# Performance work log

Hardware: AMD Instinct MI355X
Metric: run time of the kernel (lower is better)

The kernel has to match this reference:

```python
import jax, jax.numpy as jnp
import numpy as np

N_ENT = 15000  # entity id range; also used for relation ids in this synthetic setup

def _triple_key(h, r, t):
    # Unique int64 key per (h, r, t) triple; max ~15000^3 < 2^63.
    return (h * N_ENT + r) * N_ENT + t

def setup_inputs() -> dict:
    key = jax.random.key(0)
    k1, k2, k3, k4 = jax.random.split(key, 4)
    Q, N = 100000, 10000000
    heads = jax.random.randint(k1, (Q,), 0, N_ENT, dtype=jnp.int64)
    rels = jax.random.randint(k2, (Q,), 0, N_ENT, dtype=jnp.int64)
    tails = jax.random.randint(k3, (Q,), 0, N_ENT, dtype=jnp.int64)
    data = jax.random.randint(k4, (3, N), 0, N_ENT, dtype=jnp.int64)
    return {"heads": heads, "rels": rels, "tails": tails, "data": data}

def reference(heads, rels, tails, data) -> jnp.ndarray:
    # Faithful to PerfeCT.forward: response[i] = 1 iff (heads[i], rels[i], tails[i])
    # appears as a row of data.T; output = 10 * (response - 0.5).
    data_keys = jnp.sort(_triple_key(data[0], data[1], data[2]))  # [N]
    q_keys = _triple_key(heads, rels, tails)                       # [Q]
    idx = jnp.searchsorted(data_keys, q_keys)
    idx = jnp.clip(idx, 0, data_keys.shape[0] - 1)
    member = (data_keys[idx] == q_keys).astype(jnp.float32)        # [Q]
    return 10.0 * (member - 0.5)
```

## Files before the change

### kernel.cpp

```cpp
#include <hip/hip_runtime.h>
#include <stdint.h>


typedef int iv4 __attribute__((ext_vector_type(4)));

#define EMPTY 0xFFFFFFFFu

static __device__ __forceinline__ uint32_t mix32(uint32_t x) {
    x ^= x >> 16; x *= 0x85ebca6bu;
    x ^= x >> 13; x *= 0xc2b2ae35u;
    x ^= x >> 16;
    return x;
}
static __device__ __forceinline__ uint32_t hash2(uint32_t x) {
    return mix32(x ^ 0x9E3779B9u);
}
static __device__ __forceinline__ uint32_t key32(int h, int r, int t) {
    return ((uint32_t)h * 15000u + (uint32_t)r) * 15000u + (uint32_t)t;
}

__global__ void k_zero(uint32_t* __restrict__ p, int zeroWords, int totalWords) {
    int stride = gridDim.x * blockDim.x;
    for (int i = blockIdx.x * blockDim.x + threadIdx.x; i < totalWords; i += stride)
        p[i] = (i < zeroWords) ? 0u : EMPTY;
}

__global__ void k_insert(const int* __restrict__ qh, const int* __restrict__ qr,
                         const int* __restrict__ qt,
                         uint32_t* __restrict__ bloom, uint32_t* __restrict__ keys,
                         uint32_t* __restrict__ sent,
                         uint32_t bmask, uint32_t tmask, int Q) {
    int i = blockIdx.x * blockDim.x + threadIdx.x;
    if (i >= Q) return;
    uint32_t key = key32(qh[i], qr[i], qt[i]);
    if (key == EMPTY) return;
    uint32_t b = mix32(key) & bmask;
    atomicOr(&bloom[b >> 5], 1u << (b & 31));
    uint32_t slot = hash2(key) & tmask;
    while (true) {
        uint32_t prev = atomicCAS(&keys[slot], EMPTY, key);
        if (prev == EMPTY || prev == key) return;
        slot = (slot + 1) & tmask;
    }
}

static __device__ __forceinline__ void probe_mark(uint32_t key,
                                                  const uint32_t* __restrict__ keys,
                                                  uint32_t* __restrict__ flagbits,
                                                  uint32_t tmask) {
    uint32_t slot = hash2(key) & tmask;
    while (true) {
        uint32_t v = keys[slot];
        if (v == key) { atomicOr(&flagbits[slot >> 5], 1u << (slot & 31)); return; }
        if (v == EMPTY) return;
        slot = (slot + 1) & tmask;
    }
}

__global__ void k_scan(const int* __restrict__ dh, const int* __restrict__ dr,
                       const int* __restrict__ dt,
                       const uint32_t* __restrict__ bloom,
                       const uint32_t* __restrict__ keys,
                       uint32_t* __restrict__ flagbits, uint32_t* __restrict__ sent,
                       uint32_t bmask, uint32_t tmask, int nquad, int N) {
    int stride = gridDim.x * blockDim.x;
    for (int j = blockIdx.x * blockDim.x + threadIdx.x; j < nquad; j += stride) {
        iv4 h4 = ((const iv4*)dh)[j];
        iv4 r4 = ((const iv4*)dr)[j];
        iv4 t4 = ((const iv4*)dt)[j];
        uint32_t k0 = key32(h4.x, r4.x, t4.x);
        uint32_t k1 = key32(h4.y, r4.y, t4.y);
        uint32_t k2 = key32(h4.z, r4.z, t4.z);
        uint32_t k3 = key32(h4.w, r4.w, t4.w);
        uint32_t b0 = mix32(k0) & bmask, b1 = mix32(k1) & bmask;
        uint32_t b2 = mix32(k2) & bmask, b3 = mix32(k3) & bmask;
        uint32_t w0 = bloom[b0 >> 5];
        uint32_t w1 = bloom[b1 >> 5];
        uint32_t w2 = bloom[b2 >> 5];
        uint32_t w3 = bloom[b3 >> 5];
        if (k0 == EMPTY) *sent = 1u; else if ((w0 >> (b0 & 31)) & 1u) probe_mark(k0, keys, flagbits, tmask);
        if (k1 == EMPTY) *sent = 1u; else if ((w1 >> (b1 & 31)) & 1u) probe_mark(k1, keys, flagbits, tmask);
        if (k2 == EMPTY) *sent = 1u; else if ((w2 >> (b2 & 31)) & 1u) probe_mark(k2, keys, flagbits, tmask);
        if (k3 == EMPTY) *sent = 1u; else if ((w3 >> (b3 & 31)) & 1u) probe_mark(k3, keys, flagbits, tmask);
    }
    int tail = N & 3;
    if (tail && blockIdx.x == 0 && threadIdx.x < (unsigned)tail) {
        int j = N - 1 - (int)threadIdx.x;
        uint32_t k = key32(dh[j], dr[j], dt[j]);
        if (k == EMPTY) *sent = 1u;
        else probe_mark(k, keys, flagbits, tmask);
    }
}

__global__ void k_out(const int* __restrict__ qh, const int* __restrict__ qr,
                      const int* __restrict__ qt,
                      const uint32_t* __restrict__ keys,
                      const uint32_t* __restrict__ flagbits,
                      const uint32_t* __restrict__ sent,
                      float* __restrict__ out, uint32_t tmask, int Q) {
    int i = blockIdx.x * blockDim.x + threadIdx.x;
    if (i >= Q) return;
    uint32_t key = key32(qh[i], qr[i], qt[i]);
    float v = -5.0f;
    if (key == EMPTY) {
        v = (*sent) ? 5.0f : -5.0f;
    } else {
        uint32_t slot = hash2(key) & tmask;
        while (true) {
            uint32_t kv = keys[slot];
            if (kv == key) { v = ((flagbits[slot >> 5] >> (slot & 31)) & 1u) ? 5.0f : -5.0f; break; }
            if (kv == EMPTY) break;
            slot = (slot + 1) & tmask;
        }
    }
    out[i] = v;
}

extern "C" void kernel_launch(void* const* d_in, const int* in_sizes, int n_in,
                              void* d_out, int out_size, void* d_ws, size_t ws_size,
                              hipStream_t stream) {
    const int* qh = (const int*)d_in[0];
    const int* qr = (const int*)d_in[1];
    const int* qt = (const int*)d_in[2];
    const int* data = (const int*)d_in[3];
    int Q = in_sizes[0];
    int N = in_sizes[3] / 3;
    const int* dh = data;
    const int* dr = data + (size_t)N;
    const int* dt = data + 2 * (size_t)N;
    float* out = (float*)d_out;

    int bb = 22, tb = 19;
    size_t need = ((size_t)1 << (bb - 3)) + ((size_t)1 << (tb - 3)) + 256 + ((size_t)4 << tb);
    if (need > ws_size) { bb = 21; tb = 18;
        need = ((size_t)1 << (bb - 3)) + ((size_t)1 << (tb - 3)) + 256 + ((size_t)4 << tb); }
    if (need > ws_size) { bb = 20; tb = 18; }
    size_t bloomB = (size_t)1 << (bb - 3);
    size_t flagB  = (size_t)1 << (tb - 3);
    uint32_t bmask = ((uint32_t)1 << bb) - 1u;
    uint32_t tmask = ((uint32_t)1 << tb) - 1u;

    uint32_t* bloom    = (uint32_t*)d_ws;
    uint32_t* flagbits = (uint32_t*)((char*)d_ws + bloomB);
    uint32_t* sent     = (uint32_t*)((char*)d_ws + bloomB + flagB);
    uint32_t* keys     = (uint32_t*)((char*)d_ws + bloomB + flagB + 256);

    int zeroWords  = (int)((bloomB + flagB + 256) / 4);
    int totalWords = zeroWords + (1 << tb);
    k_zero<<<2048, 256, 0, stream>>>((uint32_t*)d_ws, zeroWords, totalWords);

    int qblocks = (Q + 255) / 256;
    k_insert<<<qblocks, 256, 0, stream>>>(qh, qr, qt, bloom, keys, sent, bmask, tmask, Q);

    int nquad = N / 4;
    k_scan<<<2048, 256, 0, stream>>>(dh, dr, dt, bloom, keys, flagbits, sent,
                                     bmask, tmask, nquad, N);

    k_out<<<qblocks, 256, 0, stream>>>(qh, qr, qt, keys, flagbits, sent, out, tmask, Q);
}
```

Baseline: 238.1 us.

## Use a compact LDS-resident blocked Bloom filter with two bits per key

Shrinks the Bloom filter to 32K words (128 KB) and uses a blocked two-bit-per-key test inside one word, so each block of the scan kernel copies the filter into LDS and does its lookups there instead of making random global reads. The scan kernel now runs 256 blocks of 1024 threads with launch bounds, and the hash table drops to 2^18 slots. In exchange the smaller filter gives a higher false-positive rate, so more probes reach the hash table, and every block pays for the LDS fill. The large LDS footprint also limits occupancy.

```diff
diff --git a/kernel.cpp b/kernel.cpp
--- a/kernel.cpp
+++ b/kernel.cpp
@@ -5,6 +5,7 @@
 typedef int iv4 __attribute__((ext_vector_type(4)));
 
 #define EMPTY 0xFFFFFFFFu
+#define BWORDS 32768
 
 static __device__ __forceinline__ uint32_t mix32(uint32_t x) {
     x ^= x >> 16; x *= 0x85ebca6bu;
@@ -18,6 +19,11 @@
 static __device__ __forceinline__ uint32_t key32(int h, int r, int t) {
     return ((uint32_t)h * 15000u + (uint32_t)r) * 15000u + (uint32_t)t;
 }
+static __device__ __forceinline__ void bloom_wm(uint32_t key, uint32_t* w, uint32_t* m) {
+    uint32_t z = mix32(key);
+    *w = z & (BWORDS - 1u);
+    *m = (1u << ((z >> 15) & 31u)) | (1u << ((z >> 20) & 31u));
+}
 
 __global__ void k_zero(uint32_t* __restrict__ p, int zeroWords, int totalWords) {
     int stride = gridDim.x * blockDim.x;
@@ -28,14 +34,13 @@
 __global__ void k_insert(const int* __restrict__ qh, const int* __restrict__ qr,
                          const int* __restrict__ qt,
                          uint32_t* __restrict__ bloom, uint32_t* __restrict__ keys,
-                         uint32_t* __restrict__ sent,
-                         uint32_t bmask, uint32_t tmask, int Q) {
+                         uint32_t tmask, int Q) {
     int i = blockIdx.x * blockDim.x + threadIdx.x;
     if (i >= Q) return;
     uint32_t key = key32(qh[i], qr[i], qt[i]);
     if (key == EMPTY) return;
-    uint32_t b = mix32(key) & bmask;
-    atomicOr(&bloom[b >> 5], 1u << (b & 31));
+    uint32_t w, m; bloom_wm(key, &w, &m);
+    atomicOr(&bloom[w], m);
     uint32_t slot = hash2(key) & tmask;
     while (true) {
         uint32_t prev = atomicCAS(&keys[slot], EMPTY, key);
@@ -57,12 +62,17 @@
     }
 }
 
-__global__ void k_scan(const int* __restrict__ dh, const int* __restrict__ dr,
-                       const int* __restrict__ dt,
-                       const uint32_t* __restrict__ bloom,
-                       const uint32_t* __restrict__ keys,
-                       uint32_t* __restrict__ flagbits, uint32_t* __restrict__ sent,
-                       uint32_t bmask, uint32_t tmask, int nquad, int N) {
+__global__ __launch_bounds__(1024) void k_scan(
+        const int* __restrict__ dh, const int* __restrict__ dr,
+        const int* __restrict__ dt,
+        const uint32_t* __restrict__ bloom,
+        const uint32_t* __restrict__ keys,
+        uint32_t* __restrict__ flagbits, uint32_t* __restrict__ sent,
+        uint32_t tmask, int nquad, int N) {
+    __shared__ uint32_t lb[BWORDS];
+    for (int i = threadIdx.x; i < BWORDS; i += 1024) lb[i] = bloom[i];
+    __syncthreads();
+
     int stride = gridDim.x * blockDim.x;
     for (int j = blockIdx.x * blockDim.x + threadIdx.x; j < nquad; j += stride) {
         iv4 h4 = ((const iv4*)dh)[j];
@@ -72,16 +82,14 @@
         uint32_t k1 = key32(h4.y, r4.y, t4.y);
         uint32_t k2 = key32(h4.z, r4.z, t4.z);
         uint32_t k3 = key32(h4.w, r4.w, t4.w);
-        uint32_t b0 = mix32(k0) & bmask, b1 = mix32(k1) & bmask;
-        uint32_t b2 = mix32(k2) & bmask, b3 = mix32(k3) & bmask;
-        uint32_t w0 = bloom[b0 >> 5];
-        uint32_t w1 = bloom[b1 >> 5];
-        uint32_t w2 = bloom[b2 >> 5];
-        uint32_t w3 = bloom[b3 >> 5];
-        if (k0 == EMPTY) *sent = 1u; else if ((w0 >> (b0 & 31)) & 1u) probe_mark(k0, keys, flagbits, tmask);
-        if (k1 == EMPTY) *sent = 1u; else if ((w1 >> (b1 & 31)) & 1u) probe_mark(k1, keys, flagbits, tmask);
-        if (k2 == EMPTY) *sent = 1u; else if ((w2 >> (b2 & 31)) & 1u) probe_mark(k2, keys, flagbits, tmask);
-        if (k3 == EMPTY) *sent = 1u; else if ((w3 >> (b3 & 31)) & 1u) probe_mark(k3, keys, flagbits, tmask);
+        uint32_t w0, m0, w1, m1, w2, m2, w3, m3;
+        bloom_wm(k0, &w0, &m0); bloom_wm(k1, &w1, &m1);
+        bloom_wm(k2, &w2, &m2); bloom_wm(k3, &w3, &m3);
+        uint32_t v0 = lb[w0], v1 = lb[w1], v2 = lb[w2], v3 = lb[w3];
+        if (k0 == EMPTY) *sent = 1u; else if ((v0 & m0) == m0) probe_mark(k0, keys, flagbits, tmask);
+        if (k1 == EMPTY) *sent = 1u; else if ((v1 & m1) == m1) probe_mark(k1, keys, flagbits, tmask);
+        if (k2 == EMPTY) *sent = 1u; else if ((v2 & m2) == m2) probe_mark(k2, keys, flagbits, tmask);
+        if (k3 == EMPTY) *sent = 1u; else if ((v3 & m3) == m3) probe_mark(k3, keys, flagbits, tmask);
     }
     int tail = N & 3;
     if (tail && blockIdx.x == 0 && threadIdx.x < (unsigned)tail) {
@@ -130,14 +138,11 @@
     const int* dt = data + 2 * (size_t)N;
     float* out = (float*)d_out;
 
-    int bb = 22, tb = 19;
-    size_t need = ((size_t)1 << (bb - 3)) + ((size_t)1 << (tb - 3)) + 256 + ((size_t)4 << tb);
-    if (need > ws_size) { bb = 21; tb = 18;
-        need = ((size_t)1 << (bb - 3)) + ((size_t)1 << (tb - 3)) + 256 + ((size_t)4 << tb); }
-    if (need > ws_size) { bb = 20; tb = 18; }
-    size_t bloomB = (size_t)1 << (bb - 3);
-    size_t flagB  = (size_t)1 << (tb - 3);
-    uint32_t bmask = ((uint32_t)1 << bb) - 1u;
+    int tb = 18;
+    size_t bloomB = (size_t)BWORDS * 4;
+    size_t need = bloomB + ((size_t)1 << (tb - 3)) + 256 + ((size_t)4 << tb);
+    if (need > ws_size) tb = 17;
+    size_t flagB = (size_t)1 << (tb - 3);
     uint32_t tmask = ((uint32_t)1 << tb) - 1u;
 
     uint32_t* bloom    = (uint32_t*)d_ws;
@@ -147,14 +152,14 @@
 
     int zeroWords  = (int)((bloomB + flagB + 256) / 4);
     int totalWords = zeroWords + (1 << tb);
-    k_zero<<<2048, 256, 0, stream>>>((uint32_t*)d_ws, zeroWords, totalWords);
+    k_zero<<<1024, 256, 0, stream>>>((uint32_t*)d_ws, zeroWords, totalWords);
 
     int qblocks = (Q + 255) / 256;
-    k_insert<<<qblocks, 256, 0, stream>>>(qh, qr, qt, bloom, keys, sent, bmask, tmask, Q);
+    k_insert<<<qblocks, 256, 0, stream>>>(qh, qr, qt, bloom, keys, tmask, Q);
 
     int nquad = N / 4;
-    k_scan<<<2048, 256, 0, stream>>>(dh, dr, dt, bloom, keys, flagbits, sent,
-                                     bmask, tmask, nquad, N);
+    k_scan<<<256, 1024, 0, stream>>>(dh, dr, dt, bloom, keys, flagbits, sent,
+                                     tmask, nquad, N);
 
     k_out<<<qblocks, 256, 0, stream>>>(qh, qr, qt, keys, flagbits, sent, out, tmask, Q);
 }
```

Result: no change. 235.8 us (-1.0%).
